# Kernel optimization log

Measured on AMD Instinct MI355X. Metric: run time of the kernel, lower is better.

## Reference

```python
import jax, jax.numpy as jnp
import numpy as np

DEGREE = 3
S_PNTS = 8          # sampling_points along polynomial
NUM_POINTS = 2      # deformable offsets per sampling point
S_SCALE = 0.077
SPATIAL = [(80, 80), (40, 40), (20, 20), (10, 10)]  # (h, w) per level
STARTS = [0, 6400, 8000, 8400]


def _lambdas():
    lam = jnp.linspace(0.0, 1.0, S_PNTS, dtype=jnp.float32)
    return jnp.stack([lam ** i for i in range(DEGREE, -1, -1)], 1)  # (S, degree+1)


def grid_sample_bilinear(img, grid):
    """torch F.grid_sample(mode=bilinear, padding_mode=zeros, align_corners=False).
    img: (B, C, H, W); grid: (B, Q, S, 2) with (x, y) in [-1, 1]. Returns (B, Q, S, C)."""
    B, C, H, W = img.shape
    gx = (grid[..., 0] + 1.0) * 0.5 * W - 0.5
    gy = (grid[..., 1] + 1.0) * 0.5 * H - 0.5
    x0 = jnp.floor(gx); y0 = jnp.floor(gy)
    x1 = x0 + 1.0;      y1 = y0 + 1.0
    wx1 = gx - x0; wx0 = 1.0 - wx1
    wy1 = gy - y0; wy0 = 1.0 - wy1
    flat = img.transpose(0, 2, 3, 1).reshape(B, H * W, C)  # (B, HW, C)
    Q, S = grid.shape[1], grid.shape[2]

    def fetch(xi, yi):
        valid = (xi >= 0) & (xi <= W - 1) & (yi >= 0) & (yi <= H - 1)
        xc = jnp.clip(xi, 0, W - 1).astype(jnp.int32)
        yc = jnp.clip(yi, 0, H - 1).astype(jnp.int32)
        idx = (yc * W + xc).reshape(B, Q * S, 1)
        vals = jnp.take_along_axis(flat, idx, axis=1).reshape(B, Q, S, C)
        return vals * valid[..., None].astype(img.dtype)

    out = (wy0 * wx0)[..., None] * fetch(x0, y0) \
        + (wy0 * wx1)[..., None] * fetch(x1, y0) \
        + (wy1 * wx0)[..., None] * fetch(x0, y1) \
        + (wy1 * wx1)[..., None] * fetch(x1, y1)
    return out  # (B, Q, S, C)


def setup_inputs() -> dict:
    key = jax.random.key(0)
    ks = jax.random.split(key, 6)
    B, Q, C = 8, 500, 256
    ref_polys = jax.random.uniform(ks[0], (B, Q, 2 * (DEGREE + 1)), dtype=jnp.float32)
    ref_levels = jax.random.randint(ks[1], (B, Q), 0, len(SPATIAL), dtype=jnp.int32)
    memory = jax.random.normal(ks[2], (B, 8500, C), dtype=jnp.float32)
    W1 = jax.random.normal(ks[3], (C, C), dtype=jnp.float32) * (1.0 / np.sqrt(C))
    b1 = jnp.zeros((C,), jnp.float32)
    W2 = jax.random.normal(ks[4], (C, 2 * NUM_POINTS), dtype=jnp.float32) * (1.0 / np.sqrt(C))
    b2 = jnp.zeros((2 * NUM_POINTS,), jnp.float32)
    return {"ref_polys": ref_polys, "ref_levels": ref_levels, "memory": memory,
            "W1": W1, "b1": b1, "W2": W2, "b2": b2}


def reference(ref_polys, ref_levels, memory, W1, b1, W2, b2):
    B, Q, _ = ref_polys.shape
    C = memory.shape[-1]
    lambdas = _lambdas()  # (S, degree+1)
    # polynomial evaluation: (B,Q,2,deg+1) @ (deg+1,S) -> (B,Q,S,2), mapped to [-1,1]
    rp = jax.lax.stop_gradient(ref_polys).reshape(B, Q, 2, DEGREE + 1)
    sampling_pts = 2.0 * (jnp.einsum('bqcd,sd->bqsc', rp, lambdas) - 0.5)  # (B,Q,S,2)
    # per-level bilinear sampling; memory slices reshaped to (B,C,h,w)
    sampled = []
    for (h, w), st in zip(SPATIAL, STARTS):
        lvl = memory[:, st:st + h * w, :].transpose(0, 2, 1).reshape(B, C, h, w)
        sampled.append(grid_sample_bilinear(lvl, sampling_pts))
    sampled = jnp.stack(sampled, 1)  # (B, L, Q, S, C)
    # gather the level assigned to each query
    idx = jnp.broadcast_to(ref_levels[:, None, :, None, None].astype(jnp.int32),
                           (B, 1, Q, S_PNTS, C))
    emb = jnp.take_along_axis(sampled, idx, axis=1)[:, 0]  # (B, Q, S, C)
    # 2-layer tanh MLP offset head
    h = jnp.tanh(emb @ W1 + b1)
    off = h @ W2 + b2  # (B, Q, S, 2*NUM_POINTS)
    off = S_SCALE * jnp.tanh(off.reshape(B, Q, S_PNTS, NUM_POINTS, 2))
    ref_points = off + sampling_pts[:, :, :, None, :]  # (B,Q,S,NP,2)
    return ref_points.reshape(B, Q, S_PNTS * NUM_POINTS, 2)
```

## Files before the change

### kernel.cpp

```cpp
#include <hip/hip_runtime.h>
#include <math.h>

#define S_PNTS 8
#define NUM_POINTS 2
#define NB 8
#define NQ 500
#define NC 256
#define S_SCALE 0.077f
#define QPB 4
#define ROWS (QPB * S_PNTS)
#define APAD 264

typedef __bf16 bf16x8 __attribute__((ext_vector_type(8)));
typedef __bf16 bf16x2 __attribute__((ext_vector_type(2)));
typedef float  f32x4  __attribute__((ext_vector_type(4)));

__global__ __launch_bounds__(256) void prep_w1(const float* __restrict__ W1,
                                               __bf16* __restrict__ W1t) {
    __shared__ float tile[16][17];
    const int n0 = blockIdx.x * 16, k0 = blockIdx.y * 16;
    const int tx = threadIdx.x & 15, ty = threadIdx.x >> 4;
    tile[ty][tx] = W1[(k0 + ty) * NC + n0 + tx];
    __syncthreads();
    W1t[(n0 + ty) * NC + k0 + tx] = (__bf16)tile[tx][ty];
}

__global__ __launch_bounds__(256) void decoder_kernel(
    const float* __restrict__ ref_polys,
    const int*   __restrict__ ref_levels,
    const float* __restrict__ memory,
    const __bf16* __restrict__ W1t,
    const float* __restrict__ b1,
    const float* __restrict__ W2,
    const float* __restrict__ b2,
    float*       __restrict__ out)
{
    const int tid = threadIdx.x;

    __shared__ __bf16 emb_lds[ROWS * APAD];
    __shared__ float  w2t[4 * 260];
    __shared__ float  b1_lds[NC];
    __shared__ int4   p_idx[ROWS];
    __shared__ float4 p_w[ROWS];
    __shared__ float2 spts_lds[ROWS];

    if (tid < ROWS) {
        const int r = tid, s = r & 7;
        const int qg = blockIdx.x * QPB + (r >> 3);
        const int b  = qg / NQ;
        const int lvl = ref_levels[qg];
        const int sizes[4]  = {80, 40, 20, 10};
        const int starts[4] = {0, 6400, 8000, 8400};
        const int W = sizes[lvl], st = starts[lvl];
        const float* rp = ref_polys + (size_t)qg * 8;
        float lam = (float)s * (1.0f / 7.0f);
        float sx = 2.0f * ((((rp[0] * lam + rp[1]) * lam + rp[2]) * lam + rp[3]) - 0.5f);
        float sy = 2.0f * ((((rp[4] * lam + rp[5]) * lam + rp[6]) * lam + rp[7]) - 0.5f);
        spts_lds[r] = make_float2(sx, sy);
        float gx = (sx + 1.0f) * 0.5f * (float)W - 0.5f;
        float gy = (sy + 1.0f) * 0.5f * (float)W - 0.5f;
        float x0f = floorf(gx), y0f = floorf(gy);
        int   x0 = (int)x0f,    y0 = (int)y0f;
        float wx1 = gx - x0f, wx0 = 1.0f - wx1;
        float wy1 = gy - y0f, wy0 = 1.0f - wy1;
        float xv0 = (x0 >= 0 && x0 < W) ? 1.0f : 0.0f;
        float xv1 = (x0 + 1 >= 0 && x0 + 1 < W) ? 1.0f : 0.0f;
        float yv0 = (y0 >= 0 && y0 < W) ? 1.0f : 0.0f;
        float yv1 = (y0 + 1 >= 0 && y0 + 1 < W) ? 1.0f : 0.0f;
        int xc0 = min(max(x0, 0), W - 1),     xc1 = min(max(x0 + 1, 0), W - 1);
        int yc0 = min(max(y0, 0), W - 1),     yc1 = min(max(y0 + 1, 0), W - 1);
        int base = b * 8500 + st;
        p_idx[r] = make_int4(base + yc0 * W + xc0, base + yc0 * W + xc1,
                             base + yc1 * W + xc0, base + yc1 * W + xc1);
        p_w[r] = make_float4(wy0 * wx0 * yv0 * xv0, wy0 * wx1 * yv0 * xv1,
                             wy1 * wx0 * yv1 * xv0, wy1 * wx1 * yv1 * xv1);
    }
    #pragma unroll
    for (int i = tid; i < NC * 4; i += 256) {
        int k = i >> 2, j = i & 3;
        w2t[j * 260 + k] = W2[i];
    }
    b1_lds[tid] = b1[tid];
    __syncthreads();

    {
        const int p  = tid >> 7;
        const int c2 = tid & 127;
        const float2* m2 = (const float2*)memory;
        #pragma unroll
        for (int i = 0; i < 16; ++i) {
            int r = i * 2 + p;
            int4   id = p_idx[r];
            float4 wv = p_w[r];
            float2 v00 = m2[(size_t)id.x * 128 + c2];
            float2 v01 = m2[(size_t)id.y * 128 + c2];
            float2 v10 = m2[(size_t)id.z * 128 + c2];
            float2 v11 = m2[(size_t)id.w * 128 + c2];
            float ex = wv.x * v00.x + wv.y * v01.x + wv.z * v10.x + wv.w * v11.x;
            float ey = wv.x * v00.y + wv.y * v01.y + wv.z * v10.y + wv.w * v11.y;
            bf16x2 e2; e2[0] = (__bf16)ex; e2[1] = (__bf16)ey;
            *(bf16x2*)&emb_lds[r * APAD + c2 * 2] = e2;
        }
    }
    __syncthreads();

    const int w    = tid >> 6;
    const int l    = tid & 63;
    const int lrow = l & 15;
    const int quad = l >> 4;

    f32x4 acc[2][4] = {};
    #pragma unroll
    for (int ks = 0; ks < 8; ++ks) {
        bf16x8 a0 = *(const bf16x8*)&emb_lds[(lrow)      * APAD + ks * 32 + quad * 8];
        bf16x8 a1 = *(const bf16x8*)&emb_lds[(16 + lrow) * APAD + ks * 32 + quad * 8];
        #pragma unroll
        for (int nt = 0; nt < 4; ++nt) {
            const int n = w * 64 + nt * 16 + lrow;
            bf16x8 bf = *(const bf16x8*)&W1t[n * NC + ks * 32 + quad * 8];
            acc[0][nt] = __builtin_amdgcn_mfma_f32_16x16x32_bf16(a0, bf, acc[0][nt], 0, 0, 0);
            acc[1][nt] = __builtin_amdgcn_mfma_f32_16x16x32_bf16(a1, bf, acc[1][nt], 0, 0, 0);
        }
    }
    __syncthreads();

    #pragma unroll
    for (int mt = 0; mt < 2; ++mt) {
        #pragma unroll
        for (int nt = 0; nt < 4; ++nt) {
            const int n = w * 64 + nt * 16 + lrow;
            const float bias = b1_lds[n];
            #pragma unroll
            for (int rg = 0; rg < 4; ++rg) {
                const int row = mt * 16 + quad * 4 + rg;
                emb_lds[row * APAD + n] = (__bf16)tanhf(acc[mt][nt][rg] + bias);
            }
        }
    }
    __syncthreads();

    {
        const int r    = tid >> 3;
        const int j    = (tid >> 1) & 3;
        const int half = tid & 1;
        float sum = 0.0f;
        const int kbase = half * 128;
        #pragma unroll
        for (int i = 0; i < 16; ++i) {
            const int k = kbase + i * 8;
            bf16x8 hv = *(const bf16x8*)&emb_lds[r * APAD + k];
            f32x4 wa = *(const f32x4*)&w2t[j * 260 + k];
            f32x4 wb = *(const f32x4*)&w2t[j * 260 + k + 4];
            sum += (float)hv[0] * wa[0] + (float)hv[1] * wa[1]
                 + (float)hv[2] * wa[2] + (float)hv[3] * wa[3]
                 + (float)hv[4] * wb[0] + (float)hv[5] * wb[1]
                 + (float)hv[6] * wb[2] + (float)hv[7] * wb[3];
        }
        sum += __shfl_xor(sum, 1);
        if (half == 0) {
            float o = S_SCALE * tanhf(sum + b2[j]);
            const int s = r & 7;
            const int qg = blockIdx.x * QPB + (r >> 3);
            const int np = j >> 1, coord = j & 1;
            float sp = (coord == 0) ? spts_lds[r].x : spts_lds[r].y;
            out[(size_t)qg * 32 + s * 4 + np * 2 + coord] = o + sp;
        }
    }
}

extern "C" void kernel_launch(void* const* d_in, const int* in_sizes, int n_in,
                              void* d_out, int out_size, void* d_ws, size_t ws_size,
                              hipStream_t stream) {
    const float* ref_polys  = (const float*)d_in[0];
    const int*   ref_levels = (const int*)d_in[1];
    const float* memory     = (const float*)d_in[2];
    const float* W1         = (const float*)d_in[3];
    const float* b1         = (const float*)d_in[4];
    const float* W2         = (const float*)d_in[5];
    const float* b2         = (const float*)d_in[6];
    float* out = (float*)d_out;

    __bf16* W1t = (__bf16*)d_ws;

    prep_w1<<<dim3(16, 16), dim3(256), 0, stream>>>(W1, W1t);
    decoder_kernel<<<dim3(NB * NQ / QPB), dim3(256), 0, stream>>>(
        ref_polys, ref_levels, memory, W1t, b1, W2, b2, out);
}
```

Before: 138.0 us.

## Double queries per block, widen gathers, use fast tanh approximation

Each block now handles 8 queries (64 rows) instead of 4, so every W1t fragment loaded from global memory feeds four MFMA row tiles instead of two. The bilinear gather switches from float2 to float4 loads. The libm tanhf is replaced with an exp2/rcp approximation in both layers. The second-layer dot product is restructured to one thread per output with no shuffle. The trade-offs are more accumulator registers, fewer blocks (500 instead of 1000), and slightly lower tanh precision.

New measurement: 126.5 us. -8.3%, faster.

```diff
diff --git a/kernel.cpp b/kernel.cpp
--- a/kernel.cpp
+++ b/kernel.cpp
@@ -7,13 +7,19 @@
 #define NQ 500
 #define NC 256
 #define S_SCALE 0.077f
-#define QPB 4
+#define QPB 8
 #define ROWS (QPB * S_PNTS)
 #define APAD 264
 
 typedef __bf16 bf16x8 __attribute__((ext_vector_type(8)));
-typedef __bf16 bf16x2 __attribute__((ext_vector_type(2)));
+typedef __bf16 bf16x4 __attribute__((ext_vector_type(4)));
 typedef float  f32x4  __attribute__((ext_vector_type(4)));
+
+__device__ __forceinline__ float fast_tanh(float x) {
+    float xc = fminf(fmaxf(x, -14.0f), 14.0f);
+    float t  = __builtin_amdgcn_exp2f(xc * 2.88539008178f);
+    return 1.0f - 2.0f * __builtin_amdgcn_rcpf(t + 1.0f);
+}
 
 __global__ __launch_bounds__(256) void prep_w1(const float* __restrict__ W1,
                                                __bf16* __restrict__ W1t) {
@@ -49,9 +55,8 @@
         const int qg = blockIdx.x * QPB + (r >> 3);
         const int b  = qg / NQ;
         const int lvl = ref_levels[qg];
-        const int sizes[4]  = {80, 40, 20, 10};
-        const int starts[4] = {0, 6400, 8000, 8400};
-        const int W = sizes[lvl], st = starts[lvl];
+        const int W  = 80 >> lvl;
+        const int st = (lvl >= 1) * 6400 + (lvl >= 2) * 1600 + (lvl >= 3) * 400;
         const float* rp = ref_polys + (size_t)qg * 8;
         float lam = (float)s * (1.0f / 7.0f);
         float sx = 2.0f * ((((rp[0] * lam + rp[1]) * lam + rp[2]) * lam + rp[3]) - 0.5f);
@@ -84,22 +89,24 @@
     __syncthreads();
 
     {
-        const int p  = tid >> 7;
-        const int c2 = tid & 127;
-        const float2* m2 = (const float2*)memory;
+        const int c4  = tid & 63;
+        const int rg0 = tid >> 6;
+        const float4* m4 = (const float4*)memory;
         #pragma unroll
         for (int i = 0; i < 16; ++i) {
-            int r = i * 2 + p;
+            int r = i * 4 + rg0;
             int4   id = p_idx[r];
             float4 wv = p_w[r];
-            float2 v00 = m2[(size_t)id.x * 128 + c2];
-            float2 v01 = m2[(size_t)id.y * 128 + c2];
-            float2 v10 = m2[(size_t)id.z * 128 + c2];
-            float2 v11 = m2[(size_t)id.w * 128 + c2];
-            float ex = wv.x * v00.x + wv.y * v01.x + wv.z * v10.x + wv.w * v11.x;
-            float ey = wv.x * v00.y + wv.y * v01.y + wv.z * v10.y + wv.w * v11.y;
-            bf16x2 e2; e2[0] = (__bf16)ex; e2[1] = (__bf16)ey;
-            *(bf16x2*)&emb_lds[r * APAD + c2 * 2] = e2;
+            float4 v00 = m4[(size_t)id.x * 64 + c4];
+            float4 v01 = m4[(size_t)id.y * 64 + c4];
+            float4 v10 = m4[(size_t)id.z * 64 + c4];
+            float4 v11 = m4[(size_t)id.w * 64 + c4];
+            bf16x4 e;
+            e[0] = (__bf16)(wv.x * v00.x + wv.y * v01.x + wv.z * v10.x + wv.w * v11.x);
+            e[1] = (__bf16)(wv.x * v00.y + wv.y * v01.y + wv.z * v10.y + wv.w * v11.y);
+            e[2] = (__bf16)(wv.x * v00.z + wv.y * v01.z + wv.z * v10.z + wv.w * v11.z);
+            e[3] = (__bf16)(wv.x * v00.w + wv.y * v01.w + wv.z * v10.w + wv.w * v11.w);
+            *(bf16x4*)&emb_lds[r * APAD + c4 * 4] = e;
         }
     }
     __syncthreads();
@@ -109,23 +116,26 @@
     const int lrow = l & 15;
     const int quad = l >> 4;
 
-    f32x4 acc[2][4] = {};
+    f32x4 acc[4][4] = {};
     #pragma unroll
     for (int ks = 0; ks < 8; ++ks) {
-        bf16x8 a0 = *(const bf16x8*)&emb_lds[(lrow)      * APAD + ks * 32 + quad * 8];
-        bf16x8 a1 = *(const bf16x8*)&emb_lds[(16 + lrow) * APAD + ks * 32 + quad * 8];
+        bf16x8 a[4];
+        #pragma unroll
+        for (int mt = 0; mt < 4; ++mt)
+            a[mt] = *(const bf16x8*)&emb_lds[(mt * 16 + lrow) * APAD + ks * 32 + quad * 8];
         #pragma unroll
         for (int nt = 0; nt < 4; ++nt) {
             const int n = w * 64 + nt * 16 + lrow;
             bf16x8 bf = *(const bf16x8*)&W1t[n * NC + ks * 32 + quad * 8];
-            acc[0][nt] = __builtin_amdgcn_mfma_f32_16x16x32_bf16(a0, bf, acc[0][nt], 0, 0, 0);
-            acc[1][nt] = __builtin_amdgcn_mfma_f32_16x16x32_bf16(a1, bf, acc[1][nt], 0, 0, 0);
+            #pragma unroll
+            for (int mt = 0; mt < 4; ++mt)
+                acc[mt][nt] = __builtin_amdgcn_mfma_f32_16x16x32_bf16(a[mt], bf, acc[mt][nt], 0, 0, 0);
         }
     }
     __syncthreads();
 
     #pragma unroll
-    for (int mt = 0; mt < 2; ++mt) {
+    for (int mt = 0; mt < 4; ++mt) {
         #pragma unroll
         for (int nt = 0; nt < 4; ++nt) {
             const int n = w * 64 + nt * 16 + lrow;
@@ -133,21 +143,19 @@
             #pragma unroll
             for (int rg = 0; rg < 4; ++rg) {
                 const int row = mt * 16 + quad * 4 + rg;
-                emb_lds[row * APAD + n] = (__bf16)tanhf(acc[mt][nt][rg] + bias);
+                emb_lds[row * APAD + n] = (__bf16)fast_tanh(acc[mt][nt][rg] + bias);
             }
         }
     }
     __syncthreads();
 
     {
-        const int r    = tid >> 3;
-        const int j    = (tid >> 1) & 3;
-        const int half = tid & 1;
-        float sum = 0.0f;
-        const int kbase = half * 128;
+        const int r = tid >> 2;
+        const int j = tid & 3;
+        float sum = b2[j];
         #pragma unroll
-        for (int i = 0; i < 16; ++i) {
-            const int k = kbase + i * 8;
+        for (int i = 0; i < 32; ++i) {
+            const int k = i * 8;
             bf16x8 hv = *(const bf16x8*)&emb_lds[r * APAD + k];
             f32x4 wa = *(const f32x4*)&w2t[j * 260 + k];
             f32x4 wb = *(const f32x4*)&w2t[j * 260 + k + 4];
@@ -156,15 +164,12 @@
                  + (float)hv[4] * wb[0] + (float)hv[5] * wb[1]
                  + (float)hv[6] * wb[2] + (float)hv[7] * wb[3];
         }
-        sum += __shfl_xor(sum, 1);
-        if (half == 0) {
-            float o = S_SCALE * tanhf(sum + b2[j]);
-            const int s = r & 7;
-            const int qg = blockIdx.x * QPB + (r >> 3);
-            const int np = j >> 1, coord = j & 1;
-            float sp = (coord == 0) ? spts_lds[r].x : spts_lds[r].y;
-            out[(size_t)qg * 32 + s * 4 + np * 2 + coord] = o + sp;
-        }
+        float o = S_SCALE * fast_tanh(sum);
+        const int s  = r & 7;
+        const int qg = blockIdx.x * QPB + (r >> 3);
+        const int coord = j & 1;
+        float sp = (coord == 0) ? spts_lds[r].x : spts_lds[r].y;
+        out[(size_t)qg * 32 + s * 4 + j] = o + sp;
     }
 }
 
```
